# Optimization experiments

Hardware: AMD Instinct MI355X
Metric: run time of the kernel (lower is better)

Reference implementation:

```python
import jax, jax.numpy as jnp
import numpy as np

N_NODES = 10000
N_EDGES = 320000
IN_FEATS = 128
HIDDEN = 128
NUM_CLASSES = 64


def setup_inputs() -> dict:
    key = jax.random.key(0)
    ks = jax.random.split(key, 16)
    edge_feats = jax.random.normal(ks[0], (N_EDGES, IN_FEATS), dtype=jnp.float32)
    src = jax.random.randint(ks[1], (N_EDGES,), 0, N_NODES, dtype=jnp.int32)
    dst = jax.random.randint(ks[2], (N_EDGES,), 0, N_NODES, dtype=jnp.int32)
    # guarantee every node has at least one in-edge (mean is well-defined)
    dst = dst.at[:N_NODES].set(jnp.arange(N_NODES, dtype=jnp.int32))
    def lin(k, fan_out, fan_in):
        s = 1.0 / np.sqrt(fan_in)
        kw, kb = jax.random.split(k)
        W = jax.random.uniform(kw, (fan_out, fan_in), jnp.float32, -s, s)
        b = jax.random.uniform(kb, (fan_out,), jnp.float32, -s, s)
        return W, b
    W1, b1 = lin(ks[3], HIDDEN, IN_FEATS)
    W2, b2 = lin(ks[4], HIDDEN, HIDDEN)
    W3, b3 = lin(ks[5], HIDDEN, HIDDEN)
    W4, b4 = lin(ks[6], HIDDEN, HIDDEN)
    W5, b5 = lin(ks[7], NUM_CLASSES, HIDDEN)
    return dict(edge_feats=edge_feats, src=src, dst=dst,
                W1=W1, b1=b1, W2=W2, b2=b2, W3=W3, b3=b3, W4=W4, b4=b4, W5=W5, b5=b5)


def _gcn_layer(edge_h, W, b, src, dst, in_deg):
    # (1) node h = mean of incoming edge features
    node_h = jax.ops.segment_sum(edge_h, dst, num_segments=N_NODES) / in_deg[:, None]
    # (2) send/recv: node h = sum over in-edges of src node h
    node_h = jax.ops.segment_sum(node_h[src], dst, num_segments=N_NODES)
    # (3) edge h = mean of endpoint node features
    edge_h = (node_h[src] + node_h[dst]) * 0.5
    # (4) dense linear on edge features
    return edge_h @ W.T + b


def reference(edge_feats, src, dst, W1, b1, W2, b2, W3, b3, W4, b4, W5, b5):
    in_deg = jax.ops.segment_sum(jnp.ones((N_EDGES,), jnp.float32), dst,
                                 num_segments=N_NODES)
    h = jax.nn.relu(_gcn_layer(edge_feats, W1, b1, src, dst, in_deg))
    h = jax.nn.relu(_gcn_layer(h, W2, b2, src, dst, in_deg))
    h = jax.nn.relu(_gcn_layer(h, W3, b3, src, dst, in_deg))
    h = jax.nn.relu(_gcn_layer(h, W4, b4, src, dst, in_deg))
    return _gcn_layer(h, W5, b5, src, dst, in_deg)
```

## Files before the change

kernel.cpp:

```cpp
#include <hip/hip_runtime.h>

#define NN 10000
#define NE 320000
#define F  128
#define BLK 256
#define CAP 96

__device__ __forceinline__ float bf2f(unsigned v16) {
    return __uint_as_float(v16 << 16);
}
__device__ __forceinline__ unsigned f2bf(float f) {
    unsigned u = __float_as_uint(f);
    return (u + 0x7FFFu + ((u >> 16) & 1u)) >> 16;
}
__device__ __forceinline__ unsigned pack2(float lo, float hi) {
    return f2bf(lo) | (f2bf(hi) << 16);
}
__device__ __forceinline__ void unpack8(uint4 q, float* v) {
    v[0] = bf2f(q.x & 0xffffu); v[1] = bf2f(q.x >> 16);
    v[2] = bf2f(q.y & 0xffffu); v[3] = bf2f(q.y >> 16);
    v[4] = bf2f(q.z & 0xffffu); v[5] = bf2f(q.z >> 16);
    v[6] = bf2f(q.w & 0xffffu); v[7] = bf2f(q.w >> 16);
}

__global__ void bucket_fill(const int* __restrict__ dst, const int* __restrict__ src,
                            int* __restrict__ cnt, int* __restrict__ buck,
                            int* __restrict__ bucksrc) {
    int e = blockIdx.x * 256 + threadIdx.x;
    if (e < NE) {
        int d = dst[e];
        int p = atomicAdd(&cnt[d], 1);
        buck[d * CAP + p]    = e;
        bucksrc[d * CAP + p] = src[e];
    }
}

__global__ __launch_bounds__(256) void seg_mean_k(const float4* __restrict__ ef,
                                                  const int* __restrict__ buck,
                                                  const int* __restrict__ cnt,
                                                  ushort4* __restrict__ Out) {
    __shared__ float4 red[8][32];
    int t  = threadIdx.x;
    int ns = t >> 7, es = (t >> 5) & 3, ch = t & 31;
    int n  = blockIdx.x * 2 + ns;
    int a = n * CAP, bnd = a + cnt[n];

    float ax = 0.f, ay = 0.f, az = 0.f, aw = 0.f;
    int i = a + es;
    for (; i + 28 < bnd; i += 32) {
        int s0 = buck[i],      s1 = buck[i + 4],  s2 = buck[i + 8],  s3 = buck[i + 12];
        int s4 = buck[i + 16], s5 = buck[i + 20], s6 = buck[i + 24], s7 = buck[i + 28];
        float4 v0 = ef[(size_t)s0 * 32 + ch];
        float4 v1 = ef[(size_t)s1 * 32 + ch];
        float4 v2 = ef[(size_t)s2 * 32 + ch];
        float4 v3 = ef[(size_t)s3 * 32 + ch];
        float4 v4 = ef[(size_t)s4 * 32 + ch];
        float4 v5 = ef[(size_t)s5 * 32 + ch];
        float4 v6 = ef[(size_t)s6 * 32 + ch];
        float4 v7 = ef[(size_t)s7 * 32 + ch];
        ax += v0.x + v1.x + v2.x + v3.x + v4.x + v5.x + v6.x + v7.x;
        ay += v0.y + v1.y + v2.y + v3.y + v4.y + v5.y + v6.y + v7.y;
        az += v0.z + v1.z + v2.z + v3.z + v4.z + v5.z + v6.z + v7.z;
        aw += v0.w + v1.w + v2.w + v3.w + v4.w + v5.w + v6.w + v7.w;
    }
    for (; i < bnd; i += 4) {
        float4 v0 = ef[(size_t)buck[i] * 32 + ch];
        ax += v0.x; ay += v0.y; az += v0.z; aw += v0.w;
    }

    red[(t >> 5)][ch] = make_float4(ax, ay, az, aw);
    __syncthreads();
    if (t < 64) {
        int ns2 = t >> 5, c2 = t & 31;
        float4 r0 = red[ns2 * 4 + 0][c2];
        float4 r1 = red[ns2 * 4 + 1][c2];
        float4 r2 = red[ns2 * 4 + 2][c2];
        float4 r3 = red[ns2 * 4 + 3][c2];
        int n2 = blockIdx.x * 2 + ns2;
        float sc = 1.0f / (float)cnt[n2];
        ushort4 o;
        o.x = (unsigned short)f2bf((r0.x + r1.x + r2.x + r3.x) * sc);
        o.y = (unsigned short)f2bf((r0.y + r1.y + r2.y + r3.y) * sc);
        o.z = (unsigned short)f2bf((r0.z + r1.z + r2.z + r3.z) * sc);
        o.w = (unsigned short)f2bf((r0.w + r1.w + r2.w + r3.w) * sc);
        Out[(size_t)n2 * 32 + c2] = o;
    }
}

__global__ __launch_bounds__(256) void relu_gather_k(const uint4* __restrict__ T,
                                                     const int* __restrict__ bucksrc,
                                                     const int* __restrict__ cnt,
                                                     const float* __restrict__ bias,
                                                     uint4* __restrict__ Out) {
    int t  = threadIdx.x;
    int nd = t >> 6;
    int lane = t & 63;
    int ch = lane & 15;
    int es = lane >> 4;
    int n  = blockIdx.x * 4 + nd;
    int a = n * CAP, bnd = a + cnt[n];

    float zn[8], bb[8], acc[8];
    unpack8(T[(size_t)n * 16 + ch], zn);
#pragma unroll
    for (int j = 0; j < 8; ++j) { bb[j] = bias[ch * 8 + j]; acc[j] = 0.f; }

    int i = a + es;
    for (; i + 28 < bnd; i += 32) {
        int s0 = bucksrc[i],      s1 = bucksrc[i + 4],  s2 = bucksrc[i + 8],  s3 = bucksrc[i + 12];
        int s4 = bucksrc[i + 16], s5 = bucksrc[i + 20], s6 = bucksrc[i + 24], s7 = bucksrc[i + 28];
        uint4 q0 = T[(size_t)s0 * 16 + ch];
        uint4 q1 = T[(size_t)s1 * 16 + ch];
        uint4 q2 = T[(size_t)s2 * 16 + ch];
        uint4 q3 = T[(size_t)s3 * 16 + ch];
        uint4 q4 = T[(size_t)s4 * 16 + ch];
        uint4 q5 = T[(size_t)s5 * 16 + ch];
        uint4 q6 = T[(size_t)s6 * 16 + ch];
        uint4 q7 = T[(size_t)s7 * 16 + ch];
        float v[8];
        unpack8(q0, v);
#pragma unroll
        for (int j = 0; j < 8; ++j) acc[j] += fmaxf(0.5f * (v[j] + zn[j]) + bb[j], 0.f);
        unpack8(q1, v);
#pragma unroll
        for (int j = 0; j < 8; ++j) acc[j] += fmaxf(0.5f * (v[j] + zn[j]) + bb[j], 0.f);
        unpack8(q2, v);
#pragma unroll
        for (int j = 0; j < 8; ++j) acc[j] += fmaxf(0.5f * (v[j] + zn[j]) + bb[j], 0.f);
        unpack8(q3, v);
#pragma unroll
        for (int j = 0; j < 8; ++j) acc[j] += fmaxf(0.5f * (v[j] + zn[j]) + bb[j], 0.f);
        unpack8(q4, v);
#pragma unroll
        for (int j = 0; j < 8; ++j) acc[j] += fmaxf(0.5f * (v[j] + zn[j]) + bb[j], 0.f);
        unpack8(q5, v);
#pragma unroll
        for (int j = 0; j < 8; ++j) acc[j] += fmaxf(0.5f * (v[j] + zn[j]) + bb[j], 0.f);
        unpack8(q6, v);
#pragma unroll
        for (int j = 0; j < 8; ++j) acc[j] += fmaxf(0.5f * (v[j] + zn[j]) + bb[j], 0.f);
        unpack8(q7, v);
#pragma unroll
        for (int j = 0; j < 8; ++j) acc[j] += fmaxf(0.5f * (v[j] + zn[j]) + bb[j], 0.f);
    }
    for (; i < bnd; i += 4) {
        uint4 q = T[(size_t)bucksrc[i] * 16 + ch];
        float v[8];
        unpack8(q, v);
#pragma unroll
        for (int j = 0; j < 8; ++j) acc[j] += fmaxf(0.5f * (v[j] + zn[j]) + bb[j], 0.f);
    }

#pragma unroll
    for (int j = 0; j < 8; ++j) {
        acc[j] += __shfl_xor(acc[j], 16, 64);
        acc[j] += __shfl_xor(acc[j], 32, 64);
    }

    if (es == 0) {
        float sc = 1.0f / (float)cnt[n];
        uint4 o;
        o.x = pack2(acc[0] * sc, acc[1] * sc);
        o.y = pack2(acc[2] * sc, acc[3] * sc);
        o.z = pack2(acc[4] * sc, acc[5] * sc);
        o.w = pack2(acc[6] * sc, acc[7] * sc);
        Out[(size_t)n * 16 + ch] = o;
    }
}

template <int OUT>
__global__ __launch_bounds__(256) void sum_gemm_k(const uint4* __restrict__ T,
                                                  const int* __restrict__ bucksrc,
                                                  const int* __restrict__ cnt,
                                                  const float* __restrict__ Wm,
                                                  unsigned short* __restrict__ Z) {
    __shared__ float xs[4][128];
    int t  = threadIdx.x;
    int nd = t >> 6;
    int lane = t & 63;
    int ch = lane & 15;
    int es = lane >> 4;
    int n  = blockIdx.x * 4 + nd;
    int a = n * CAP, bnd = a + cnt[n];

    float acc[8];
#pragma unroll
    for (int j = 0; j < 8; ++j) acc[j] = 0.f;

    int i = a + es;
    for (; i + 28 < bnd; i += 32) {
        int s0 = bucksrc[i],      s1 = bucksrc[i + 4],  s2 = bucksrc[i + 8],  s3 = bucksrc[i + 12];
        int s4 = bucksrc[i + 16], s5 = bucksrc[i + 20], s6 = bucksrc[i + 24], s7 = bucksrc[i + 28];
        uint4 q0 = T[(size_t)s0 * 16 + ch];
        uint4 q1 = T[(size_t)s1 * 16 + ch];
        uint4 q2 = T[(size_t)s2 * 16 + ch];
        uint4 q3 = T[(size_t)s3 * 16 + ch];
        uint4 q4 = T[(size_t)s4 * 16 + ch];
        uint4 q5 = T[(size_t)s5 * 16 + ch];
        uint4 q6 = T[(size_t)s6 * 16 + ch];
        uint4 q7 = T[(size_t)s7 * 16 + ch];
        float v[8];
        unpack8(q0, v);
#pragma unroll
        for (int j = 0; j < 8; ++j) acc[j] += v[j];
        unpack8(q1, v);
#pragma unroll
        for (int j = 0; j < 8; ++j) acc[j] += v[j];
        unpack8(q2, v);
#pragma unroll
        for (int j = 0; j < 8; ++j) acc[j] += v[j];
        unpack8(q3, v);
#pragma unroll
        for (int j = 0; j < 8; ++j) acc[j] += v[j];
        unpack8(q4, v);
#pragma unroll
        for (int j = 0; j < 8; ++j) acc[j] += v[j];
        unpack8(q5, v);
#pragma unroll
        for (int j = 0; j < 8; ++j) acc[j] += v[j];
        unpack8(q6, v);
#pragma unroll
        for (int j = 0; j < 8; ++j) acc[j] += v[j];
        unpack8(q7, v);
#pragma unroll
        for (int j = 0; j < 8; ++j) acc[j] += v[j];
    }
    for (; i < bnd; i += 4) {
        uint4 q = T[(size_t)bucksrc[i] * 16 + ch];
        float v[8];
        unpack8(q, v);
#pragma unroll
        for (int j = 0; j < 8; ++j) acc[j] += v[j];
    }

#pragma unroll
    for (int j = 0; j < 8; ++j) {
        acc[j] += __shfl_xor(acc[j], 16, 64);
        acc[j] += __shfl_xor(acc[j], 32, 64);
    }
    if (es == 0) {
#pragma unroll
        for (int j = 0; j < 8; ++j) xs[nd][ch * 8 + j] = acc[j];
    }
    __syncthreads();

    if (t < OUT) {
        const float4* wrow = reinterpret_cast<const float4*>(&Wm[(size_t)t * 128]);
        float a0 = 0.f, a1 = 0.f, a2 = 0.f, a3 = 0.f;
#pragma unroll 8
        for (int k4 = 0; k4 < 32; ++k4) {
            float4 w  = wrow[k4];
            float4 x0 = *reinterpret_cast<const float4*>(&xs[0][k4 * 4]);
            float4 x1 = *reinterpret_cast<const float4*>(&xs[1][k4 * 4]);
            float4 x2 = *reinterpret_cast<const float4*>(&xs[2][k4 * 4]);
            float4 x3 = *reinterpret_cast<const float4*>(&xs[3][k4 * 4]);
            a0 += w.x * x0.x + w.y * x0.y + w.z * x0.z + w.w * x0.w;
            a1 += w.x * x1.x + w.y * x1.y + w.z * x1.z + w.w * x1.w;
            a2 += w.x * x2.x + w.y * x2.y + w.z * x2.z + w.w * x2.w;
            a3 += w.x * x3.x + w.y * x3.y + w.z * x3.z + w.w * x3.w;
        }
        int nb = blockIdx.x * 4;
        Z[(size_t)(nb + 0) * OUT + t] = (unsigned short)f2bf(a0);
        Z[(size_t)(nb + 1) * OUT + t] = (unsigned short)f2bf(a1);
        Z[(size_t)(nb + 2) * OUT + t] = (unsigned short)f2bf(a2);
        Z[(size_t)(nb + 3) * OUT + t] = (unsigned short)f2bf(a3);
    }
}

__global__ __launch_bounds__(256) void edge_out(const uint4* __restrict__ z5,
                                                const float* __restrict__ b5,
                                                const int* __restrict__ src,
                                                const int* __restrict__ dst,
                                                float4* __restrict__ outp) {
    int t = blockIdx.x * 256 + threadIdx.x;
    int e = t >> 3, ch = t & 7;
    if (e < NE) {
        float va[8], vb[8];
        unpack8(z5[(size_t)src[e] * 8 + ch], va);
        unpack8(z5[(size_t)dst[e] * 8 + ch], vb);
        float4 r0, r1;
        r0.x = 0.5f * (va[0] + vb[0]) + b5[ch * 8 + 0];
        r0.y = 0.5f * (va[1] + vb[1]) + b5[ch * 8 + 1];
        r0.z = 0.5f * (va[2] + vb[2]) + b5[ch * 8 + 2];
        r0.w = 0.5f * (va[3] + vb[3]) + b5[ch * 8 + 3];
        r1.x = 0.5f * (va[4] + vb[4]) + b5[ch * 8 + 4];
        r1.y = 0.5f * (va[5] + vb[5]) + b5[ch * 8 + 5];
        r1.z = 0.5f * (va[6] + vb[6]) + b5[ch * 8 + 6];
        r1.w = 0.5f * (va[7] + vb[7]) + b5[ch * 8 + 7];
        outp[(size_t)e * 16 + ch * 2 + 0] = r0;
        outp[(size_t)e * 16 + ch * 2 + 1] = r1;
    }
}

extern "C" void kernel_launch(void* const* d_in, const int* in_sizes, int n_in,
                              void* d_out, int out_size, void* d_ws, size_t ws_size,
                              hipStream_t stream) {
    const float* ef  = (const float*)d_in[0];
    const int*   src = (const int*)d_in[1];
    const int*   dst = (const int*)d_in[2];
    const float* W1 = (const float*)d_in[3];  const float* b1 = (const float*)d_in[4];
    const float* W2 = (const float*)d_in[5];  const float* b2 = (const float*)d_in[6];
    const float* W3 = (const float*)d_in[7];  const float* b3 = (const float*)d_in[8];
    const float* W4 = (const float*)d_in[9];  const float* b4 = (const float*)d_in[10];
    const float* W5 = (const float*)d_in[11]; const float* b5 = (const float*)d_in[12];
    float* out = (float*)d_out;

    char* p = (char*)d_ws;
    auto alloc = [&](size_t bytes) {
        char* r = p;
        p += (bytes + 255) & ~(size_t)255;
        return r;
    };
    int* cnt     = (int*)alloc(NN * 4);
    int* buck    = (int*)alloc((size_t)NN * CAP * 4);
    int* bucksrc = (int*)alloc((size_t)NN * CAP * 4);
    unsigned short* m = (unsigned short*)alloc((size_t)NN * F * 2);
    unsigned short* z = (unsigned short*)alloc((size_t)NN * F * 2);

    hipMemsetAsync(cnt, 0, NN * 4, stream);
    bucket_fill<<<(NE + 255) / 256, 256, 0, stream>>>(dst, src, cnt, buck, bucksrc);

    const int G2 = NN / 2;
    const int G4 = NN / 4;
    const uint4* m4 = (const uint4*)m;
    const uint4* z4 = (const uint4*)z;

    seg_mean_k<<<G2, BLK, 0, stream>>>((const float4*)ef, buck, cnt, (ushort4*)m);
    sum_gemm_k<128><<<G4, BLK, 0, stream>>>(m4, bucksrc, cnt, W1, z);

    const float* Wl[3] = {W2, W3, W4};
    const float* bl[3] = {b1, b2, b3};
    for (int L = 0; L < 3; ++L) {
        relu_gather_k<<<G4, BLK, 0, stream>>>(z4, bucksrc, cnt, bl[L], (uint4*)m);
        sum_gemm_k<128><<<G4, BLK, 0, stream>>>(m4, bucksrc, cnt, Wl[L], z);
    }

    relu_gather_k<<<G4, BLK, 0, stream>>>(z4, bucksrc, cnt, b4, (uint4*)m);
    sum_gemm_k<64><<<G4, BLK, 0, stream>>>(m4, bucksrc, cnt, W5, z);

    edge_out<<<(NE * 8 + 255) / 256, BLK, 0, stream>>>(z4, b5, src, dst, (float4*)out);
}
```

Measured before the change: 286.2 us.

## Remap gather kernels to fewer lanes per node with deeper unrolled loads

The edge-to-node mean kernel now gives each node a single 64-lane wave and reduces with one cross-lane shuffle, replacing the shared-memory reduction and block barrier. The relu-gather and sum-gemm kernels pack two nodes per wave (32 lanes each) and run 128-thread blocks. A shared macro unrolls 16 outstanding row loads per lane to raise memory-level parallelism. The output kernel becomes a grid-stride loop over a fixed grid. The intent is to cut reduction and sync overhead and keep more loads in flight, at the cost of higher register pressure and less parallelism per node for nodes with many edges.

```diff
diff --git a/kernel.cpp b/kernel.cpp
--- a/kernel.cpp
+++ b/kernel.cpp
@@ -3,7 +3,6 @@
 #define NN 10000
 #define NE 320000
 #define F  128
-#define BLK 256
 #define CAP 96
 
 __device__ __forceinline__ float bf2f(unsigned v16) {
@@ -39,17 +38,18 @@
                                                   const int* __restrict__ buck,
                                                   const int* __restrict__ cnt,
                                                   ushort4* __restrict__ Out) {
-    __shared__ float4 red[8][32];
-    int t  = threadIdx.x;
-    int ns = t >> 7, es = (t >> 5) & 3, ch = t & 31;
-    int n  = blockIdx.x * 2 + ns;
+    int t    = threadIdx.x;
+    int lane = t & 63;
+    int ch   = lane & 31;
+    int slot = lane >> 5;
+    int n    = blockIdx.x * 4 + (t >> 6);
     int a = n * CAP, bnd = a + cnt[n];
 
     float ax = 0.f, ay = 0.f, az = 0.f, aw = 0.f;
-    int i = a + es;
-    for (; i + 28 < bnd; i += 32) {
-        int s0 = buck[i],      s1 = buck[i + 4],  s2 = buck[i + 8],  s3 = buck[i + 12];
-        int s4 = buck[i + 16], s5 = buck[i + 20], s6 = buck[i + 24], s7 = buck[i + 28];
+    int i = a + slot;
+    for (; i + 14 < bnd; i += 16) {
+        int s0 = buck[i],      s1 = buck[i + 2],  s2 = buck[i + 4],  s3 = buck[i + 6];
+        int s4 = buck[i + 8],  s5 = buck[i + 10], s6 = buck[i + 12], s7 = buck[i + 14];
         float4 v0 = ef[(size_t)s0 * 32 + ch];
         float4 v1 = ef[(size_t)s1 * 32 + ch];
         float4 v2 = ef[(size_t)s2 * 32 + ch];
@@ -63,41 +63,67 @@
         az += v0.z + v1.z + v2.z + v3.z + v4.z + v5.z + v6.z + v7.z;
         aw += v0.w + v1.w + v2.w + v3.w + v4.w + v5.w + v6.w + v7.w;
     }
-    for (; i < bnd; i += 4) {
+    for (; i < bnd; i += 2) {
         float4 v0 = ef[(size_t)buck[i] * 32 + ch];
         ax += v0.x; ay += v0.y; az += v0.z; aw += v0.w;
     }
 
-    red[(t >> 5)][ch] = make_float4(ax, ay, az, aw);
-    __syncthreads();
-    if (t < 64) {
-        int ns2 = t >> 5, c2 = t & 31;
-        float4 r0 = red[ns2 * 4 + 0][c2];
-        float4 r1 = red[ns2 * 4 + 1][c2];
-        float4 r2 = red[ns2 * 4 + 2][c2];
-        float4 r3 = red[ns2 * 4 + 3][c2];
-        int n2 = blockIdx.x * 2 + ns2;
-        float sc = 1.0f / (float)cnt[n2];
+    ax += __shfl_xor(ax, 32, 64);
+    ay += __shfl_xor(ay, 32, 64);
+    az += __shfl_xor(az, 32, 64);
+    aw += __shfl_xor(aw, 32, 64);
+
+    if (slot == 0) {
+        float sc = 1.0f / (float)cnt[n];
         ushort4 o;
-        o.x = (unsigned short)f2bf((r0.x + r1.x + r2.x + r3.x) * sc);
-        o.y = (unsigned short)f2bf((r0.y + r1.y + r2.y + r3.y) * sc);
-        o.z = (unsigned short)f2bf((r0.z + r1.z + r2.z + r3.z) * sc);
-        o.w = (unsigned short)f2bf((r0.w + r1.w + r2.w + r3.w) * sc);
-        Out[(size_t)n2 * 32 + c2] = o;
-    }
-}
-
-__global__ __launch_bounds__(256) void relu_gather_k(const uint4* __restrict__ T,
+        o.x = (unsigned short)f2bf(ax * sc);
+        o.y = (unsigned short)f2bf(ay * sc);
+        o.z = (unsigned short)f2bf(az * sc);
+        o.w = (unsigned short)f2bf(aw * sc);
+        Out[(size_t)n * 32 + ch] = o;
+    }
+}
+
+#define GATHER16(IDX, TT, BODY)                                                         \
+    int i = a + slot;                                                                   \
+    for (; i + 30 < bnd; i += 32) {                     \
+        int s0 = IDX[i],      s1 = IDX[i + 2],  s2 = IDX[i + 4],  s3 = IDX[i + 6];      \
+        int s4 = IDX[i + 8],  s5 = IDX[i + 10], s6 = IDX[i + 12], s7 = IDX[i + 14];     \
+        int s8 = IDX[i + 16], s9 = IDX[i + 18], sA = IDX[i + 20], sB = IDX[i + 22];     \
+        int sC = IDX[i + 24], sD = IDX[i + 26], sE = IDX[i + 28], sF = IDX[i + 30];     \
+        uint4 q0 = TT[(size_t)s0 * 16 + ch], q1 = TT[(size_t)s1 * 16 + ch];             \
+        uint4 q2 = TT[(size_t)s2 * 16 + ch], q3 = TT[(size_t)s3 * 16 + ch];             \
+        uint4 q4 = TT[(size_t)s4 * 16 + ch], q5 = TT[(size_t)s5 * 16 + ch];             \
+        uint4 q6 = TT[(size_t)s6 * 16 + ch], q7 = TT[(size_t)s7 * 16 + ch];             \
+        uint4 q8 = TT[(size_t)s8 * 16 + ch], q9 = TT[(size_t)s9 * 16 + ch];             \
+        uint4 qA = TT[(size_t)sA * 16 + ch], qB = TT[(size_t)sB * 16 + ch];             \
+        uint4 qC = TT[(size_t)sC * 16 + ch], qD = TT[(size_t)sD * 16 + ch];             \
+        uint4 qE = TT[(size_t)sE * 16 + ch], qF = TT[(size_t)sF * 16 + ch];             \
+        float v[8];                                                                     \
+        unpack8(q0, v); BODY; unpack8(q1, v); BODY; unpack8(q2, v); BODY;               \
+        unpack8(q3, v); BODY; unpack8(q4, v); BODY; unpack8(q5, v); BODY;               \
+        unpack8(q6, v); BODY; unpack8(q7, v); BODY; unpack8(q8, v); BODY;               \
+        unpack8(q9, v); BODY; unpack8(qA, v); BODY; unpack8(qB, v); BODY;               \
+        unpack8(qC, v); BODY; unpack8(qD, v); BODY; unpack8(qE, v); BODY;               \
+        unpack8(qF, v); BODY;                                                           \
+    }                                                                                   \
+    for (; i < bnd; i += 2) {                                                           \
+        uint4 q = TT[(size_t)IDX[i] * 16 + ch];                                         \
+        float v[8];                                                                     \
+        unpack8(q, v); BODY;                                                            \
+    }
+
+__global__ __launch_bounds__(128) void relu_gather_k(const uint4* __restrict__ T,
                                                      const int* __restrict__ bucksrc,
                                                      const int* __restrict__ cnt,
                                                      const float* __restrict__ bias,
                                                      uint4* __restrict__ Out) {
-    int t  = threadIdx.x;
-    int nd = t >> 6;
+    int t    = threadIdx.x;
     int lane = t & 63;
-    int ch = lane & 15;
-    int es = lane >> 4;
-    int n  = blockIdx.x * 4 + nd;
+    int ch   = lane & 15;
+    int slot = (lane >> 4) & 1;
+    int half = lane >> 5;
+    int n    = blockIdx.x * 4 + (t >> 6) * 2 + half;
     int a = n * CAP, bnd = a + cnt[n];
 
     float zn[8], bb[8], acc[8];
@@ -105,59 +131,15 @@
 #pragma unroll
     for (int j = 0; j < 8; ++j) { bb[j] = bias[ch * 8 + j]; acc[j] = 0.f; }
 
-    int i = a + es;
-    for (; i + 28 < bnd; i += 32) {
-        int s0 = bucksrc[i],      s1 = bucksrc[i + 4],  s2 = bucksrc[i + 8],  s3 = bucksrc[i + 12];
-        int s4 = bucksrc[i + 16], s5 = bucksrc[i + 20], s6 = bucksrc[i + 24], s7 = bucksrc[i + 28];
-        uint4 q0 = T[(size_t)s0 * 16 + ch];
-        uint4 q1 = T[(size_t)s1 * 16 + ch];
-        uint4 q2 = T[(size_t)s2 * 16 + ch];
-        uint4 q3 = T[(size_t)s3 * 16 + ch];
-        uint4 q4 = T[(size_t)s4 * 16 + ch];
-        uint4 q5 = T[(size_t)s5 * 16 + ch];
-        uint4 q6 = T[(size_t)s6 * 16 + ch];
-        uint4 q7 = T[(size_t)s7 * 16 + ch];
-        float v[8];
-        unpack8(q0, v);
-#pragma unroll
-        for (int j = 0; j < 8; ++j) acc[j] += fmaxf(0.5f * (v[j] + zn[j]) + bb[j], 0.f);
-        unpack8(q1, v);
-#pragma unroll
-        for (int j = 0; j < 8; ++j) acc[j] += fmaxf(0.5f * (v[j] + zn[j]) + bb[j], 0.f);
-        unpack8(q2, v);
-#pragma unroll
-        for (int j = 0; j < 8; ++j) acc[j] += fmaxf(0.5f * (v[j] + zn[j]) + bb[j], 0.f);
-        unpack8(q3, v);
-#pragma unroll
-        for (int j = 0; j < 8; ++j) acc[j] += fmaxf(0.5f * (v[j] + zn[j]) + bb[j], 0.f);
-        unpack8(q4, v);
-#pragma unroll
-        for (int j = 0; j < 8; ++j) acc[j] += fmaxf(0.5f * (v[j] + zn[j]) + bb[j], 0.f);
-        unpack8(q5, v);
-#pragma unroll
-        for (int j = 0; j < 8; ++j) acc[j] += fmaxf(0.5f * (v[j] + zn[j]) + bb[j], 0.f);
-        unpack8(q6, v);
-#pragma unroll
-        for (int j = 0; j < 8; ++j) acc[j] += fmaxf(0.5f * (v[j] + zn[j]) + bb[j], 0.f);
-        unpack8(q7, v);
-#pragma unroll
-        for (int j = 0; j < 8; ++j) acc[j] += fmaxf(0.5f * (v[j] + zn[j]) + bb[j], 0.f);
-    }
-    for (; i < bnd; i += 4) {
-        uint4 q = T[(size_t)bucksrc[i] * 16 + ch];
-        float v[8];
-        unpack8(q, v);
-#pragma unroll
-        for (int j = 0; j < 8; ++j) acc[j] += fmaxf(0.5f * (v[j] + zn[j]) + bb[j], 0.f);
-    }
-
-#pragma unroll
-    for (int j = 0; j < 8; ++j) {
-        acc[j] += __shfl_xor(acc[j], 16, 64);
-        acc[j] += __shfl_xor(acc[j], 32, 64);
-    }
-
-    if (es == 0) {
+#define RELU_BODY { _Pragma("unroll") for (int j = 0; j < 8; ++j) \
+        acc[j] += fmaxf(0.5f * (v[j] + zn[j]) + bb[j], 0.f); }
+    GATHER16(bucksrc, T, RELU_BODY)
+#undef RELU_BODY
+
+#pragma unroll
+    for (int j = 0; j < 8; ++j) acc[j] += __shfl_xor(acc[j], 16, 64);
+
+    if (slot == 0) {
         float sc = 1.0f / (float)cnt[n];
         uint4 o;
         o.x = pack2(acc[0] * sc, acc[1] * sc);
@@ -169,76 +151,32 @@
 }
 
 template <int OUT>
-__global__ __launch_bounds__(256) void sum_gemm_k(const uint4* __restrict__ T,
+__global__ __launch_bounds__(128) void sum_gemm_k(const uint4* __restrict__ T,
                                                   const int* __restrict__ bucksrc,
                                                   const int* __restrict__ cnt,
                                                   const float* __restrict__ Wm,
                                                   unsigned short* __restrict__ Z) {
     __shared__ float xs[4][128];
-    int t  = threadIdx.x;
-    int nd = t >> 6;
+    int t    = threadIdx.x;
     int lane = t & 63;
-    int ch = lane & 15;
-    int es = lane >> 4;
-    int n  = blockIdx.x * 4 + nd;
+    int ch   = lane & 15;
+    int slot = (lane >> 4) & 1;
+    int half = lane >> 5;
+    int nd   = (t >> 6) * 2 + half;
+    int n    = blockIdx.x * 4 + nd;
     int a = n * CAP, bnd = a + cnt[n];
 
     float acc[8];
 #pragma unroll
     for (int j = 0; j < 8; ++j) acc[j] = 0.f;
 
-    int i = a + es;
-    for (; i + 28 < bnd; i += 32) {
-        int s0 = bucksrc[i],      s1 = bucksrc[i + 4],  s2 = bucksrc[i + 8],  s3 = bucksrc[i + 12];
-        int s4 = bucksrc[i + 16], s5 = bucksrc[i + 20], s6 = bucksrc[i + 24], s7 = bucksrc[i + 28];
-        uint4 q0 = T[(size_t)s0 * 16 + ch];
-        uint4 q1 = T[(size_t)s1 * 16 + ch];
-        uint4 q2 = T[(size_t)s2 * 16 + ch];
-        uint4 q3 = T[(size_t)s3 * 16 + ch];
-        uint4 q4 = T[(size_t)s4 * 16 + ch];
-        uint4 q5 = T[(size_t)s5 * 16 + ch];
-        uint4 q6 = T[(size_t)s6 * 16 + ch];
-        uint4 q7 = T[(size_t)s7 * 16 + ch];
-        float v[8];
-        unpack8(q0, v);
-#pragma unroll
-        for (int j = 0; j < 8; ++j) acc[j] += v[j];
-        unpack8(q1, v);
-#pragma unroll
-        for (int j = 0; j < 8; ++j) acc[j] += v[j];
-        unpack8(q2, v);
-#pragma unroll
-        for (int j = 0; j < 8; ++j) acc[j] += v[j];
-        unpack8(q3, v);
-#pragma unroll
-        for (int j = 0; j < 8; ++j) acc[j] += v[j];
-        unpack8(q4, v);
-#pragma unroll
-        for (int j = 0; j < 8; ++j) acc[j] += v[j];
-        unpack8(q5, v);
-#pragma unroll
-        for (int j = 0; j < 8; ++j) acc[j] += v[j];
-        unpack8(q6, v);
-#pragma unroll
-        for (int j = 0; j < 8; ++j) acc[j] += v[j];
-        unpack8(q7, v);
-#pragma unroll
-        for (int j = 0; j < 8; ++j) acc[j] += v[j];
-    }
-    for (; i < bnd; i += 4) {
-        uint4 q = T[(size_t)bucksrc[i] * 16 + ch];
-        float v[8];
-        unpack8(q, v);
-#pragma unroll
-        for (int j = 0; j < 8; ++j) acc[j] += v[j];
-    }
-
-#pragma unroll
-    for (int j = 0; j < 8; ++j) {
-        acc[j] += __shfl_xor(acc[j], 16, 64);
-        acc[j] += __shfl_xor(acc[j], 32, 64);
-    }
-    if (es == 0) {
+#define SUM_BODY { _Pragma("unroll") for (int j = 0; j < 8; ++j) acc[j] += v[j]; }
+    GATHER16(bucksrc, T, SUM_BODY)
+#undef SUM_BODY
+
+#pragma unroll
+    for (int j = 0; j < 8; ++j) acc[j] += __shfl_xor(acc[j], 16, 64);
+    if (slot == 0) {
 #pragma unroll
         for (int j = 0; j < 8; ++j) xs[nd][ch * 8 + j] = acc[j];
     }
@@ -272,9 +210,9 @@
                                                 const int* __restrict__ src,
                                                 const int* __restrict__ dst,
                                                 float4* __restrict__ outp) {
-    int t = blockIdx.x * 256 + threadIdx.x;
-    int e = t >> 3, ch = t & 7;
-    if (e < NE) {
+    int gs = gridDim.x * 256;
+    for (int t = blockIdx.x * 256 + threadIdx.x; t < NE * 8; t += gs) {
+        int e = t >> 3, ch = t & 7;
         float va[8], vb[8];
         unpack8(z5[(size_t)src[e] * 8 + ch], va);
         unpack8(z5[(size_t)dst[e] * 8 + ch], vb);
@@ -320,23 +258,22 @@
     hipMemsetAsync(cnt, 0, NN * 4, stream);
     bucket_fill<<<(NE + 255) / 256, 256, 0, stream>>>(dst, src, cnt, buck, bucksrc);
 
-    const int G2 = NN / 2;
     const int G4 = NN / 4;
     const uint4* m4 = (const uint4*)m;
     const uint4* z4 = (const uint4*)z;
 
-    seg_mean_k<<<G2, BLK, 0, stream>>>((const float4*)ef, buck, cnt, (ushort4*)m);
-    sum_gemm_k<128><<<G4, BLK, 0, stream>>>(m4, bucksrc, cnt, W1, z);
+    seg_mean_k<<<G4, 256, 0, stream>>>((const float4*)ef, buck, cnt, (ushort4*)m);
+    sum_gemm_k<128><<<G4, 128, 0, stream>>>(m4, bucksrc, cnt, W1, z);
 
     const float* Wl[3] = {W2, W3, W4};
     const float* bl[3] = {b1, b2, b3};
     for (int L = 0; L < 3; ++L) {
-        relu_gather_k<<<G4, BLK, 0, stream>>>(z4, bucksrc, cnt, bl[L], (uint4*)m);
-        sum_gemm_k<128><<<G4, BLK, 0, stream>>>(m4, bucksrc, cnt, Wl[L], z);
-    }
-
-    relu_gather_k<<<G4, BLK, 0, stream>>>(z4, bucksrc, cnt, b4, (uint4*)m);
-    sum_gemm_k<64><<<G4, BLK, 0, stream>>>(m4, bucksrc, cnt, W5, z);
-
-    edge_out<<<(NE * 8 + 255) / 256, BLK, 0, stream>>>(z4, b5, src, dst, (float4*)out);
-}
+        relu_gather_k<<<G4, 128, 0, stream>>>(z4, bucksrc, cnt, bl[L], (uint4*)m);
+        sum_gemm_k<128><<<G4, 128, 0, stream>>>(m4, bucksrc, cnt, Wl[L], z);
+    }
+
+    relu_gather_k<<<G4, 128, 0, stream>>>(z4, bucksrc, cnt, b4, (uint4*)m);
+    sum_gemm_k<64><<<G4, 128, 0, stream>>>(m4, bucksrc, cnt, W5, z);
+
+    edge_out<<<4096, 256, 0, stream>>>(z4, b5, src, dst, (float4*)out);
+}
```

New measurement: 318.0 us. 11.1% more time.
